# Performance work log

Measured on AMD Instinct MI355X. Metric: run time of the kernel, lower is better.

Reference implementation:

```python
import jax, jax.numpy as jnp
import numpy as np

# LocBlock.get_obj_matrix, fully vectorized over batch B and points N.
# Per point i: Q_e[c,c]=w_i*kron(m_i m_i^T, I3), Q_e[t,t]=w_i*I3,
# Q_e[h,h]=w_i*y_i^T y_i, Q_e[c,t]=-w_i*kron(m_i, I3), Q_e[c,h]=-w_i*kron(m_i, y_i),
# Q_e[t,h]=w_i*y_i; summed over i, then offset removed and Frobenius-normalized.

B, N = 1024, 4096

def setup_inputs() -> dict:
    key = jax.random.key(0)
    k1, k2, k3 = jax.random.split(key, 3)
    return {
        "keypoints_3D_src": jax.random.normal(k1, (B, 3, N), dtype=jnp.float32),
        "keypoints_3D_trg": jax.random.normal(k2, (B, 3, N), dtype=jnp.float32),
        "weights": jax.random.uniform(k3, (B, 1, N), dtype=jnp.float32),
    }


def reference(keypoints_3D_src, keypoints_3D_trg, weights):
    m = keypoints_3D_src              # (B,3,N) source points
    y = keypoints_3D_trg              # (B,3,N) target points
    w = weights[:, 0, :]              # (B,N) per-point scalar weights
    b = m.shape[0]
    I3 = jnp.eye(3, dtype=m.dtype)

    # weighted moment sums over points
    Mw = jnp.einsum('bin,bjn,bn->bij', m, m, w)          # (B,3,3) sum w m m^T
    mw = jnp.einsum('bin,bn->bi', m, w)                  # (B,3)   sum w m
    yw = jnp.einsum('bin,bn->bi', y, w)                  # (B,3)   sum w y
    MY = jnp.einsum('bin,bjn,bn->bij', m, y, w)          # (B,3,3) sum w m y^T
    sw = jnp.sum(w, axis=-1)                             # (B,)    sum w
    yy = jnp.einsum('bin,bin,bn->b', y, y, w)            # (B,)    sum w y^T y

    # assemble blocks (kron index convention: kron(A,B)[3i+k,3j+l]=A[ij]B[kl])
    Qcc = jnp.einsum('bij,kl->bikjl', Mw, I3).reshape(b, 9, 9)   # kron(Mw, I3)
    Qct = -jnp.einsum('bi,kl->bikl', mw, I3).reshape(b, 9, 3)    # -kron(mw, I3)
    Qch = -MY.reshape(b, 9)                                      # -kron(m, W y) summed
    Qtt = sw[:, None, None] * I3                                 # (B,3,3)

    Q = jnp.zeros((b, 13, 13), dtype=m.dtype)
    Q = Q.at[:, 1:10, 1:10].set(Qcc)
    Q = Q.at[:, 10:13, 10:13].set(Qtt)
    Q = Q.at[:, 1:10, 10:13].set(Qct)
    Q = Q.at[:, 10:13, 1:10].set(jnp.swapaxes(Qct, 1, 2))
    Q = Q.at[:, 1:10, 0].set(Qch)
    Q = Q.at[:, 0, 1:10].set(Qch)
    Q = Q.at[:, 10:13, 0].set(yw)
    Q = Q.at[:, 0, 10:13].set(yw)
    # Q[0,0] would be yy (offset); original zeroes it before normalization
    offsets = yy
    scales = jnp.sqrt(jnp.sum(Q * Q, axis=(1, 2)))  # Frobenius norm with Q[0,0]=0
    Qn = Q / scales[:, None, None]
    return Qn, scales, offsets
```

## Files before the change

kernel.cpp:

```cpp
#include <hip/hip_runtime.h>
#include <math.h>

#define BATCH   1024
#define NPTS    4096
#define THREADS 256
#define WAVES   (THREADS / 64)


__global__ __launch_bounds__(THREADS) void locblock_kernel(
    const float* __restrict__ m,
    const float* __restrict__ y,
    const float* __restrict__ w,
    float* __restrict__ out)
{
    const int b    = blockIdx.x;
    const int tid  = threadIdx.x;
    const int lane = tid & 63;
    const int wave = tid >> 6;

    const size_t mb = (size_t)b * 3 * NPTS;
    const float4* m0p = (const float4*)(m + mb + 0 * NPTS);
    const float4* m1p = (const float4*)(m + mb + 1 * NPTS);
    const float4* m2p = (const float4*)(m + mb + 2 * NPTS);
    const float4* y0p = (const float4*)(y + mb + 0 * NPTS);
    const float4* y1p = (const float4*)(y + mb + 1 * NPTS);
    const float4* y2p = (const float4*)(y + mb + 2 * NPTS);
    const float4* wp  = (const float4*)(w + (size_t)b * NPTS);

    float acc[23];
#pragma unroll
    for (int i = 0; i < 23; ++i) acc[i] = 0.f;

    auto accum = [&](float wv, float m0v, float m1v, float m2v,
                     float y0v, float y1v, float y2v) {
        float wm0 = wv * m0v, wm1 = wv * m1v, wm2 = wv * m2v;
        acc[0]  += wv;
        acc[1]  += wm0;        acc[2]  += wm1;        acc[3]  += wm2;
        acc[4]  += wv * y0v;   acc[5]  += wv * y1v;   acc[6]  += wv * y2v;
        acc[7]  += wm0 * m0v;  acc[8]  += wm0 * m1v;  acc[9]  += wm0 * m2v;
        acc[10] += wm1 * m1v;  acc[11] += wm1 * m2v;  acc[12] += wm2 * m2v;
        acc[13] += wm0 * y0v;  acc[14] += wm0 * y1v;  acc[15] += wm0 * y2v;
        acc[16] += wm1 * y0v;  acc[17] += wm1 * y1v;  acc[18] += wm1 * y2v;
        acc[19] += wm2 * y0v;  acc[20] += wm2 * y1v;  acc[21] += wm2 * y2v;
        acc[22] += wv * (y0v * y0v + y1v * y1v + y2v * y2v);
    };

    const int NV = NPTS / 4;
#pragma unroll
    for (int v = tid; v < NV; v += THREADS) {
        float4 M0 = m0p[v], M1 = m1p[v], M2 = m2p[v];
        float4 Y0 = y0p[v], Y1 = y1p[v], Y2 = y2p[v];
        float4 W  = wp[v];
        accum(W.x, M0.x, M1.x, M2.x, Y0.x, Y1.x, Y2.x);
        accum(W.y, M0.y, M1.y, M2.y, Y0.y, Y1.y, Y2.y);
        accum(W.z, M0.z, M1.z, M2.z, Y0.z, Y1.z, Y2.z);
        accum(W.w, M0.w, M1.w, M2.w, Y0.w, Y1.w, Y2.w);
    }

#pragma unroll
    for (int i = 0; i < 23; ++i) {
        float v = acc[i];
        v += __shfl_xor(v, 32, 64);
        v += __shfl_xor(v, 16, 64);
        v += __shfl_xor(v, 8, 64);
        v += __shfl_xor(v, 4, 64);
        v += __shfl_xor(v, 2, 64);
        v += __shfl_xor(v, 1, 64);
        acc[i] = v;
    }

    __shared__ float partial[WAVES][23];
    __shared__ float sums[23];
    __shared__ float red[WAVES];
    __shared__ float scale_s;

    if (lane == 0) {
#pragma unroll
        for (int i = 0; i < 23; ++i) partial[wave][i] = acc[i];
    }
    __syncthreads();
    if (tid < 23) {
        sums[tid] = partial[0][tid] + partial[1][tid] + partial[2][tid] + partial[3][tid];
    }
    __syncthreads();

    float qv = 0.f;
    if (tid < 169) {
        const int r = tid / 13, c = tid % 13;
        const float sw = sums[0];
        const float* mwv = &sums[1];
        const float* ywv = &sums[4];
        auto Mwf = [&](int i, int j) -> float {
            if (i > j) { int t = i; i = j; j = t; }
            int idx = (i == 0) ? j : ((i == 1) ? (j + 2) : 5);
            return sums[7 + idx];
        };
        auto MYf = [&](int i, int j) -> float { return sums[13 + i * 3 + j]; };

        if (r == 0) {
            if (c == 0)            qv = 0.f;
            else if (c <= 9)       qv = -MYf((c - 1) / 3, (c - 1) % 3);
            else                   qv = ywv[c - 10];
        } else if (c == 0) {
            if (r <= 9)            qv = -MYf((r - 1) / 3, (r - 1) % 3);
            else                   qv = ywv[r - 10];
        } else if (r <= 9 && c <= 9) {
            int a = r - 1, d = c - 1;
            int i = a / 3, k = a % 3, j = d / 3, l = d % 3;
            qv = (k == l) ? Mwf(i, j) : 0.f;
        } else if (r <= 9) {
            int a = r - 1, i = a / 3, k = a % 3, l = c - 10;
            qv = (k == l) ? -mwv[i] : 0.f;
        } else if (c <= 9) {
            int a = c - 1, i = a / 3, k = a % 3, l = r - 10;
            qv = (k == l) ? -mwv[i] : 0.f;
        } else {
            qv = (r == c) ? sums[0] : 0.f;
        }
        (void)sw;
    }

    float sq = (tid < 169) ? qv * qv : 0.f;
    sq += __shfl_xor(sq, 32, 64);
    sq += __shfl_xor(sq, 16, 64);
    sq += __shfl_xor(sq, 8, 64);
    sq += __shfl_xor(sq, 4, 64);
    sq += __shfl_xor(sq, 2, 64);
    sq += __shfl_xor(sq, 1, 64);
    if (lane == 0) red[wave] = sq;
    __syncthreads();
    if (tid == 0) {
        scale_s = sqrtf(red[0] + red[1] + red[2] + red[3]);
    }
    __syncthreads();

    const float inv_scale = 1.0f / scale_s;
    if (tid < 169) {
        out[(size_t)b * 169 + tid] = qv * inv_scale;
    }
    if (tid == 0) {
        out[(size_t)BATCH * 169 + b]         = scale_s;
        out[(size_t)BATCH * 169 + BATCH + b] = sums[22];
    }
}

extern "C" void kernel_launch(void* const* d_in, const int* in_sizes, int n_in,
                              void* d_out, int out_size, void* d_ws, size_t ws_size,
                              hipStream_t stream) {
    const float* m = (const float*)d_in[0];
    const float* y = (const float*)d_in[1];
    const float* w = (const float*)d_in[2];
    float* out = (float*)d_out;
    locblock_kernel<<<BATCH, THREADS, 0, stream>>>(m, y, w, out);
}
```

Baseline: 138.0 us.

## Split each batch's point reduction across two blocks with a finalize kernel

Splits the per-batch reduction over points into two blocks per batch element. Each block writes partial moment sums to workspace, and a second kernel combines them and assembles the normalized 13x13 matrix. Within each block, all vector loads for a thread are issued before any accumulation, so more memory requests are in flight. The aims are to raise occupancy and memory-level parallelism on the bandwidth-bound reduction. The cost is an extra kernel launch and a workspace round trip.

```diff
diff --git a/kernel.cpp b/kernel.cpp
--- a/kernel.cpp
+++ b/kernel.cpp
@@ -1,35 +1,44 @@
 #include <hip/hip_runtime.h>
 #include <math.h>
 
-#define BATCH   1024
-#define NPTS    4096
-#define THREADS 256
-#define WAVES   (THREADS / 64)
+#define BATCH    1024
+#define NPTS     4096
+#define THREADS  256
+#define WAVES    (THREADS / 64)
+#define SPLITS   2
+#define SLICE    (NPTS / SPLITS)
+#define SLICE_V  (SLICE / 4)
+#define ITERS    (SLICE_V / THREADS)
+#define NACC     23
+#define WS_STRIDE 24
 
 
-__global__ __launch_bounds__(THREADS) void locblock_kernel(
+__global__ __launch_bounds__(THREADS) void locblock_stage1(
     const float* __restrict__ m,
     const float* __restrict__ y,
     const float* __restrict__ w,
-    float* __restrict__ out)
+    float* __restrict__ ws)
 {
-    const int b    = blockIdx.x;
+    const int blk  = blockIdx.x;
+    const int b    = blk >> 1;
+    const int s    = blk & 1;
     const int tid  = threadIdx.x;
     const int lane = tid & 63;
     const int wave = tid >> 6;
 
-    const size_t mb = (size_t)b * 3 * NPTS;
-    const float4* m0p = (const float4*)(m + mb + 0 * NPTS);
-    const float4* m1p = (const float4*)(m + mb + 1 * NPTS);
-    const float4* m2p = (const float4*)(m + mb + 2 * NPTS);
-    const float4* y0p = (const float4*)(y + mb + 0 * NPTS);
-    const float4* y1p = (const float4*)(y + mb + 1 * NPTS);
-    const float4* y2p = (const float4*)(y + mb + 2 * NPTS);
-    const float4* wp  = (const float4*)(w + (size_t)b * NPTS);
+    const size_t mb  = (size_t)b * 3 * NPTS;
+    const int    off = s * SLICE;
+    const float4* m0p = (const float4*)(m + mb + 0 * NPTS + off);
+    const float4* m1p = (const float4*)(m + mb + 1 * NPTS + off);
+    const float4* m2p = (const float4*)(m + mb + 2 * NPTS + off);
+    const float4* y0p = (const float4*)(y + mb + 0 * NPTS + off);
+    const float4* y1p = (const float4*)(y + mb + 1 * NPTS + off);
+    const float4* y2p = (const float4*)(y + mb + 2 * NPTS + off);
+    const float4* wp  = (const float4*)(w + (size_t)b * NPTS + off);
 
-    float acc[23];
+    float acc[NACC];
 #pragma unroll
-    for (int i = 0; i < 23; ++i) acc[i] = 0.f;
+    for (int i = 0; i < NACC; ++i) acc[i] = 0.f;
 
     auto accum = [&](float wv, float m0v, float m1v, float m2v,
                      float y0v, float y1v, float y2v) {
@@ -45,20 +54,24 @@
         acc[22] += wv * (y0v * y0v + y1v * y1v + y2v * y2v);
     };
 
-    const int NV = NPTS / 4;
+    float4 M0[ITERS], M1[ITERS], M2[ITERS], Y0[ITERS], Y1[ITERS], Y2[ITERS], W[ITERS];
 #pragma unroll
-    for (int v = tid; v < NV; v += THREADS) {
-        float4 M0 = m0p[v], M1 = m1p[v], M2 = m2p[v];
-        float4 Y0 = y0p[v], Y1 = y1p[v], Y2 = y2p[v];
-        float4 W  = wp[v];
-        accum(W.x, M0.x, M1.x, M2.x, Y0.x, Y1.x, Y2.x);
-        accum(W.y, M0.y, M1.y, M2.y, Y0.y, Y1.y, Y2.y);
-        accum(W.z, M0.z, M1.z, M2.z, Y0.z, Y1.z, Y2.z);
-        accum(W.w, M0.w, M1.w, M2.w, Y0.w, Y1.w, Y2.w);
+    for (int it = 0; it < ITERS; ++it) {
+        const int v = it * THREADS + tid;
+        M0[it] = m0p[v]; M1[it] = m1p[v]; M2[it] = m2p[v];
+        Y0[it] = y0p[v]; Y1[it] = y1p[v]; Y2[it] = y2p[v];
+        W[it]  = wp[v];
+    }
+#pragma unroll
+    for (int it = 0; it < ITERS; ++it) {
+        accum(W[it].x, M0[it].x, M1[it].x, M2[it].x, Y0[it].x, Y1[it].x, Y2[it].x);
+        accum(W[it].y, M0[it].y, M1[it].y, M2[it].y, Y0[it].y, Y1[it].y, Y2[it].y);
+        accum(W[it].z, M0[it].z, M1[it].z, M2[it].z, Y0[it].z, Y1[it].z, Y2[it].z);
+        accum(W[it].w, M0[it].w, M1[it].w, M2[it].w, Y0[it].w, Y1[it].w, Y2[it].w);
     }
 
 #pragma unroll
-    for (int i = 0; i < 23; ++i) {
+    for (int i = 0; i < NACC; ++i) {
         float v = acc[i];
         v += __shfl_xor(v, 32, 64);
         v += __shfl_xor(v, 16, 64);
@@ -69,25 +82,43 @@
         acc[i] = v;
     }
 
-    __shared__ float partial[WAVES][23];
-    __shared__ float sums[23];
+    __shared__ float partial[WAVES][NACC];
+    if (lane == 0) {
+#pragma unroll
+        for (int i = 0; i < NACC; ++i) partial[wave][i] = acc[i];
+    }
+    __syncthreads();
+    if (tid < NACC) {
+        ws[(size_t)blk * WS_STRIDE + tid] =
+            partial[0][tid] + partial[1][tid] + partial[2][tid] + partial[3][tid];
+    }
+}
+
+__global__ __launch_bounds__(THREADS) void locblock_stage2(
+    const float* __restrict__ ws,
+    float* __restrict__ out)
+{
+    const int b    = blockIdx.x;
+    const int tid  = threadIdx.x;
+    const int lane = tid & 63;
+    const int wave = tid >> 6;
+
+    __shared__ float sums[NACC];
     __shared__ float red[WAVES];
     __shared__ float scale_s;
 
-    if (lane == 0) {
+    if (tid < NACC) {
+        float v = 0.f;
 #pragma unroll
-        for (int i = 0; i < 23; ++i) partial[wave][i] = acc[i];
-    }
-    __syncthreads();
-    if (tid < 23) {
-        sums[tid] = partial[0][tid] + partial[1][tid] + partial[2][tid] + partial[3][tid];
+        for (int s = 0; s < SPLITS; ++s)
+            v += ws[(size_t)(b * SPLITS + s) * WS_STRIDE + tid];
+        sums[tid] = v;
     }
     __syncthreads();
 
     float qv = 0.f;
     if (tid < 169) {
         const int r = tid / 13, c = tid % 13;
-        const float sw = sums[0];
         const float* mwv = &sums[1];
         const float* ywv = &sums[4];
         auto Mwf = [&](int i, int j) -> float {
@@ -117,7 +148,6 @@
         } else {
             qv = (r == c) ? sums[0] : 0.f;
         }
-        (void)sw;
     }
 
     float sq = (tid < 169) ? qv * qv : 0.f;
@@ -151,5 +181,8 @@
     const float* y = (const float*)d_in[1];
     const float* w = (const float*)d_in[2];
     float* out = (float*)d_out;
-    locblock_kernel<<<BATCH, THREADS, 0, stream>>>(m, y, w, out);
+    float* ws  = (float*)d_ws;
+
+    locblock_stage1<<<BATCH * SPLITS, THREADS, 0, stream>>>(m, y, w, ws);
+    locblock_stage2<<<BATCH, THREADS, 0, stream>>>(ws, out);
 }
```

Result: no change. 140.6 us (+1.9%).
